# Performance work log

Hardware: AMD Instinct MI355X
Metric: run time of the kernel (lower is better)

The kernel has to match this reference:

```python
import jax, jax.numpy as jnp
import numpy as np

B, N, C = 8, 4096, 768
H = 12
D = C // H  # 64


def setup_inputs() -> dict:
    key = jax.random.key(0)
    k1, k2, k3 = jax.random.split(key, 3)
    x = jax.random.normal(k1, (B, N, C), dtype=jnp.float32)
    Wqkv = jax.random.normal(k2, (C, 3 * C), dtype=jnp.float32) * (1.0 / np.sqrt(C))
    Wproj = jax.random.normal(k3, (C, C), dtype=jnp.float32) * (1.0 / np.sqrt(C))
    bproj = jnp.zeros((C,), dtype=jnp.float32)
    return {"x": x, "Wqkv": Wqkv, "Wproj": Wproj, "bproj": bproj}


def reference(x, Wqkv, Wproj, bproj):
    b, n, c = x.shape
    # qkv: [B,N,3C] -> [B,N,3,H,D] -> [3,B,H,N,D]
    qkv = (x @ Wqkv).reshape(b, n, 3, H, D).transpose(2, 0, 3, 1, 4)
    q, k, v = qkv[0], qkv[1], qkv[2]
    q = jax.nn.softmax(q, axis=-1)  # softmax over head_dim (feature map)
    k = jax.nn.softmax(k, axis=-1)
    # context: [B,H,D,D] (small per-head matrix)
    context = jnp.einsum('bhnd,bhne->bhde', k, v)
    out = jnp.einsum('bhnd,bhde->bhne', q, context)  # [B,H,N,D]
    out = out.transpose(0, 2, 1, 3).reshape(b, n, c)
    return out @ Wproj + bproj
```

## Files before the change

kernel.cpp:

```cpp
#include <hip/hip_runtime.h>

typedef unsigned short u16;
typedef unsigned int u32;
typedef __attribute__((ext_vector_type(4))) float f32x4;
typedef __attribute__((ext_vector_type(8))) short bf16x8;
typedef __attribute__((ext_vector_type(8))) u16 u16x8;

__device__ __forceinline__ u16 f2b(float f) {
  union { float f; u32 u; } v; v.f = f;
  u32 r = v.u + 0x7FFFu + ((v.u >> 16) & 1u);
  return (u16)(r >> 16);
}
__device__ __forceinline__ float b2f(u16 h) {
  union { u32 u; float f; } v; v.u = ((u32)h) << 16;
  return v.f;
}
__device__ __forceinline__ void gload_lds16(const void* g, void* lds) {
  __builtin_amdgcn_global_load_lds(
      (__attribute__((address_space(1))) void*)(void*)g,
      (__attribute__((address_space(3))) void*)lds, 16, 0, 0);
}

__global__ __launch_bounds__(256) void cast_x_kernel(const float* __restrict__ x,
                                                     u16* __restrict__ xb, size_t n8) {
  size_t i = (size_t)blockIdx.x * blockDim.x + threadIdx.x;
  size_t stride = (size_t)gridDim.x * blockDim.x;
  for (; i < n8; i += stride) {
    const float4* p = (const float4*)(x + i * 8);
    float4 a = p[0], b = p[1];
    u16x8 o;
    o[0] = f2b(a.x); o[1] = f2b(a.y); o[2] = f2b(a.z); o[3] = f2b(a.w);
    o[4] = f2b(b.x); o[5] = f2b(b.y); o[6] = f2b(b.z); o[7] = f2b(b.w);
    *(u16x8*)(xb + i * 8) = o;
  }
}

template <bool PERM>
__global__ __launch_bounds__(256) void transpose_cast_kernel(const float* __restrict__ W,
                                                             u16* __restrict__ WT,
                                                             int R, int C) {
  __shared__ u16 tile[32][33];
  int rt = R >> 5;
  int tr = blockIdx.x % rt, tc = blockIdx.x / rt;
  int r0 = tr * 32, c0 = tc * 32;
#pragma unroll
  for (int i = 0; i < 4; ++i) {
    int r = (threadIdx.x >> 5) + i * 8, c = threadIdx.x & 31;
    tile[r][c] = f2b(W[(size_t)(r0 + r) * C + c0 + c]);
  }
  __syncthreads();
#pragma unroll
  for (int i = 0; i < 4; ++i) {
    int c = (threadIdx.x >> 5) + i * 8, r = threadIdx.x & 31;
    int cc = c0 + c;
    if (PERM && cc >= 768) {
      int t = cc - 768;
      int isv = (t >= 768) ? 1 : 0;
      int tk = t - isv * 768;
      cc = 768 + (tk >> 6) * 128 + isv * 64 + (tk & 63);
    }
    WT[(size_t)cc * R + r0 + r] = tile[r][c];
  }
}

template <bool G1, bool BIAS, bool BATCHB>
__global__ __launch_bounds__(256, 4) void gemm128_kernel(
    const u16* __restrict__ A, const u16* __restrict__ BT, void* __restrict__ Cv,
    float* __restrict__ Pw, const float* __restrict__ bias, int N, int lda, int ntile) {
  constexpr int K = 768;
  constexpr int NT = 24;
  __shared__ __align__(16) u16 lds[20480];
  u16* Asb = lds;
  u16* Bsb = lds + 8192;
  const int tid = threadIdx.x;
  const int wave = tid >> 6, lane = tid & 63;
  const int lr = lane & 15, hi = lane >> 4;
  const int wr = wave >> 1, wc = wave & 1;

  const int cpx = gridDim.x >> 3;
  const int wg = (blockIdx.x & 7) * cpx + (blockIdx.x >> 3);
  const int tm = wg / ntile, tn = wg % ntile;

  const size_t rowA0 = (size_t)tm * 128;
  const size_t rowB0 = (size_t)tn * 128;
  const u16* BTb = BATCHB ? (BT + (size_t)(tm >> 5) * 589824) : BT;

  const int dby = tid * 16;
  const int sby = dby ^ (((dby >> 7) & 3) << 4);
  const int srow = sby >> 6;
  const int scol = (sby & 63) >> 1;
  const u16* pA = A + (rowA0 + srow) * (size_t)lda + scol;
  const u16* pB = BTb + (rowB0 + srow) * (size_t)K + scol;
  u16* Adst = Asb + wave * 512;
  u16* Bdst = Bsb + wave * 512;

  const int flip = ((lr >> 1) & 3) << 4;
  const int baseA = ((((wr * 64 + lr) * 64) + hi * 16) ^ flip) >> 1;
  const int baseB = ((((wc * 64 + lr) * 64) + hi * 16) ^ flip) >> 1;

  f32x4 acc[4][4] = {};

#define STG_A(tt)                                                          \
  { const u16* _s = pA + (size_t)(tt) * 32;                                \
    u16* _d = Adst + ((tt) & 1) * 4096;                                    \
    gload_lds16(_s, _d); gload_lds16(_s + (size_t)64 * lda, _d + 2048); }
#define STG_B(tt)                                                          \
  { const u16* _s = pB + (size_t)(tt) * 32;                                \
    u16* _d = Bdst + ((tt) % 3) * 4096;                                    \
    gload_lds16(_s, _d); gload_lds16(_s + (size_t)64 * K, _d + 2048); }

  STG_A(0); STG_B(0); STG_B(1);
  asm volatile("s_waitcnt vmcnt(2)" ::: "memory");
  __builtin_amdgcn_sched_barrier(0);
  __builtin_amdgcn_s_barrier();

#pragma unroll
  for (int t = 0; t < NT; ++t) {
    const u16* Ab = Asb + (t & 1) * 4096;
    const u16* Bb = Bsb + (t % 3) * 4096;
    bf16x8 a0 = *(const bf16x8*)&Ab[baseA];
    bf16x8 a1 = *(const bf16x8*)&Ab[baseA + 512];
    bf16x8 a2 = *(const bf16x8*)&Ab[baseA + 1024];
    bf16x8 a3 = *(const bf16x8*)&Ab[baseA + 1536];
    bf16x8 b0 = *(const bf16x8*)&Bb[baseB];
    bf16x8 b1 = *(const bf16x8*)&Bb[baseB + 512];
    bf16x8 b2 = *(const bf16x8*)&Bb[baseB + 1024];
    bf16x8 b3 = *(const bf16x8*)&Bb[baseB + 1536];
    if (t + 1 < NT) STG_A(t + 1);
    if (t + 2 < NT) STG_B(t + 2);
    asm volatile("s_waitcnt lgkmcnt(0)" ::: "memory");
    __builtin_amdgcn_sched_barrier(0);
    __builtin_amdgcn_s_setprio(1);
    acc[0][0] = __builtin_amdgcn_mfma_f32_16x16x32_bf16(a0, b0, acc[0][0], 0, 0, 0);
    acc[0][1] = __builtin_amdgcn_mfma_f32_16x16x32_bf16(a0, b1, acc[0][1], 0, 0, 0);
    acc[0][2] = __builtin_amdgcn_mfma_f32_16x16x32_bf16(a0, b2, acc[0][2], 0, 0, 0);
    acc[0][3] = __builtin_amdgcn_mfma_f32_16x16x32_bf16(a0, b3, acc[0][3], 0, 0, 0);
    acc[1][0] = __builtin_amdgcn_mfma_f32_16x16x32_bf16(a1, b0, acc[1][0], 0, 0, 0);
    acc[1][1] = __builtin_amdgcn_mfma_f32_16x16x32_bf16(a1, b1, acc[1][1], 0, 0, 0);
    acc[1][2] = __builtin_amdgcn_mfma_f32_16x16x32_bf16(a1, b2, acc[1][2], 0, 0, 0);
    acc[1][3] = __builtin_amdgcn_mfma_f32_16x16x32_bf16(a1, b3, acc[1][3], 0, 0, 0);
    acc[2][0] = __builtin_amdgcn_mfma_f32_16x16x32_bf16(a2, b0, acc[2][0], 0, 0, 0);
    acc[2][1] = __builtin_amdgcn_mfma_f32_16x16x32_bf16(a2, b1, acc[2][1], 0, 0, 0);
    acc[2][2] = __builtin_amdgcn_mfma_f32_16x16x32_bf16(a2, b2, acc[2][2], 0, 0, 0);
    acc[2][3] = __builtin_amdgcn_mfma_f32_16x16x32_bf16(a2, b3, acc[2][3], 0, 0, 0);
    acc[3][0] = __builtin_amdgcn_mfma_f32_16x16x32_bf16(a3, b0, acc[3][0], 0, 0, 0);
    acc[3][1] = __builtin_amdgcn_mfma_f32_16x16x32_bf16(a3, b1, acc[3][1], 0, 0, 0);
    acc[3][2] = __builtin_amdgcn_mfma_f32_16x16x32_bf16(a3, b2, acc[3][2], 0, 0, 0);
    acc[3][3] = __builtin_amdgcn_mfma_f32_16x16x32_bf16(a3, b3, acc[3][3], 0, 0, 0);
    __builtin_amdgcn_s_setprio(0);
    if (t < NT - 2) {
      asm volatile("s_waitcnt vmcnt(2)" ::: "memory");
    } else if (t == NT - 2) {
      asm volatile("s_waitcnt vmcnt(0)" ::: "memory");
    }
    __builtin_amdgcn_sched_barrier(0);
    if (t + 1 < NT) __builtin_amdgcn_s_barrier();
  }
#undef STG_A
#undef STG_B

  const int ocol0 = tn * 128 + wc * 64;
  const int orow0 = tm * 128 + wr * 64;

  if (!G1 || tn < 6) {
#pragma unroll
    for (int mf = 0; mf < 4; ++mf) {
      if (G1) {
#pragma unroll
        for (int q = 0; q < 4; ++q) {
          float v0 = acc[mf][0][q], v1 = acc[mf][1][q];
          float v2 = acc[mf][2][q], v3 = acc[mf][3][q];
          float mx = fmaxf(fmaxf(v0, v1), fmaxf(v2, v3));
#pragma unroll
          for (int s = 1; s <= 8; s <<= 1) mx = fmaxf(mx, __shfl_xor(mx, s, 64));
          float e0 = __expf(v0 - mx), e1 = __expf(v1 - mx);
          float e2 = __expf(v2 - mx), e3 = __expf(v3 - mx);
          float sm = e0 + e1 + e2 + e3;
#pragma unroll
          for (int s = 1; s <= 8; s <<= 1) sm += __shfl_xor(sm, s, 64);
          float inv = 1.0f / sm;
          acc[mf][0][q] = e0 * inv; acc[mf][1][q] = e1 * inv;
          acc[mf][2][q] = e2 * inv; acc[mf][3][q] = e3 * inv;
        }
      }
#pragma unroll
      for (int nf = 0; nf < 4; ++nf) {
        const int col = ocol0 + nf * 16 + lr;
        const float bv = BIAS ? bias[col] : 0.0f;
#pragma unroll
        for (int q = 0; q < 4; ++q) {
          const int row = orow0 + mf * 16 + hi * 4 + q;
          const float v = acc[mf][nf][q] + bv;
          if (G1) ((u16*)Cv)[(size_t)row * 768 + col] = f2b(v);
          else    ((float*)Cv)[(size_t)row * N + col] = v;
        }
      }
    }
  } else {
    const int h = tn - 6;
    if (wc == 0) {
#pragma unroll
      for (int mf = 0; mf < 4; ++mf)
#pragma unroll
        for (int q = 0; q < 4; ++q) {
          float v0 = acc[mf][0][q], v1 = acc[mf][1][q];
          float v2 = acc[mf][2][q], v3 = acc[mf][3][q];
          float mx = fmaxf(fmaxf(v0, v1), fmaxf(v2, v3));
#pragma unroll
          for (int s = 1; s <= 8; s <<= 1) mx = fmaxf(mx, __shfl_xor(mx, s, 64));
          float e0 = __expf(v0 - mx), e1 = __expf(v1 - mx);
          float e2 = __expf(v2 - mx), e3 = __expf(v3 - mx);
          float sm = e0 + e1 + e2 + e3;
#pragma unroll
          for (int s = 1; s <= 8; s <<= 1) sm += __shfl_xor(sm, s, 64);
          float inv = 1.0f / sm;
          acc[mf][0][q] = e0 * inv; acc[mf][1][q] = e1 * inv;
          acc[mf][2][q] = e2 * inv; acc[mf][3][q] = e3 * inv;
        }
    }
    __syncthreads();
    u16* kT = lds;
    u16* vT = lds + 8704;
    u16* tgt = wc ? vT : kT;
#pragma unroll
    for (int mf = 0; mf < 4; ++mf)
#pragma unroll
      for (int nf = 0; nf < 4; ++nf)
#pragma unroll
        for (int q = 0; q < 4; ++q)
          tgt[(nf * 16 + lr) * 136 + wr * 64 + mf * 16 + hi * 4 + q] =
              f2b(acc[mf][nf][q]);
    __syncthreads();
    f32x4 cacc[4] = {};
#pragma unroll
    for (int ks = 0; ks < 4; ++ks) {
      bf16x8 ak = *(const bf16x8*)&kT[(wave * 16 + lr) * 136 + ks * 32 + hi * 8];
#pragma unroll
      for (int ef = 0; ef < 4; ++ef) {
        bf16x8 bv = *(const bf16x8*)&vT[(ef * 16 + lr) * 136 + ks * 32 + hi * 8];
        cacc[ef] = __builtin_amdgcn_mfma_f32_16x16x32_bf16(ak, bv, cacc[ef], 0, 0, 0);
      }
    }
    float* dst = Pw + ((size_t)tm * 12 + h) * 4096;
#pragma unroll
    for (int ef = 0; ef < 4; ++ef)
#pragma unroll
      for (int q = 0; q < 4; ++q)
        dst[(wave * 16 + hi * 4 + q) * 64 + ef * 16 + lr] = cacc[ef][q];
  }
}

__global__ __launch_bounds__(256) void ctx_reduce_kernel(const float* __restrict__ partial,
                                                         u16* __restrict__ ctxD) {
  int idx = blockIdx.x * 256 + threadIdx.x;
  int bh = idx >> 12;
  int b = bh / 12, h = bh % 12;
  int de = idx & 4095;
  float s = 0.0f;
#pragma unroll 8
  for (int i = 0; i < 32; ++i)
    s += partial[((size_t)(b * 32 + i) * 12 + h) * 4096 + de];
  ctxD[(size_t)bh * 4096 + de] = f2b(s);
}

__global__ __launch_bounds__(256) void make_w2_kernel(const u16* __restrict__ WprojT,
                                                      const u16* __restrict__ ctxD,
                                                      u16* __restrict__ BT2) {
  __shared__ u16 qs[128 * 64];
  __shared__ u16 cs[64 * 64];
  int bid = blockIdx.x;
  int b = bid / 72, rest = bid % 72;
  int h = rest / 6, ct = rest % 6;
  int bh = b * 12 + h;
  int tid = threadIdx.x, wave = tid >> 6, lane = tid & 63;
  int lr = lane & 15, lk = (lane >> 4) << 3;
#pragma unroll
  for (int it = 0; it < 4; ++it) {
    int u = it * 256 + tid;
    int r = u >> 3, c8 = (u & 7) * 8;
    gload_lds16(WprojT + (size_t)(ct * 128 + r) * 768 + h * 64 + c8,
                &qs[(it * 256 + wave * 64) * 8]);
  }
#pragma unroll
  for (int it = 0; it < 2; ++it) {
    int u = it * 256 + tid;
    gload_lds16(ctxD + (size_t)bh * 4096 + u * 8, &cs[(it * 256 + wave * 64) * 8]);
  }
  asm volatile("s_waitcnt vmcnt(0)" ::: "memory");
  __syncthreads();
  f32x4 acc[2][4] = {};
#pragma unroll
  for (int ks = 0; ks < 2; ++ks) {
    bf16x8 bv[4];
#pragma unroll
    for (int jt = 0; jt < 4; ++jt) bv[jt] = *(const bf16x8*)&cs[(jt * 16 + lr) * 64 + ks * 32 + lk];
#pragma unroll
    for (int i = 0; i < 2; ++i) {
      bf16x8 af = *(const bf16x8*)&qs[(wave * 32 + i * 16 + lr) * 64 + ks * 32 + lk];
#pragma unroll
      for (int jt = 0; jt < 4; ++jt)
        acc[i][jt] = __builtin_amdgcn_mfma_f32_16x16x32_bf16(af, bv[jt], acc[i][jt], 0, 0, 0);
    }
  }
#pragma unroll
  for (int i = 0; i < 2; ++i)
#pragma unroll
    for (int jt = 0; jt < 4; ++jt)
#pragma unroll
      for (int q = 0; q < 4; ++q) {
        int cp = ct * 128 + wave * 32 + i * 16 + (lane >> 4) * 4 + q;
        int col = h * 64 + jt * 16 + lr;
        BT2[(size_t)b * 589824 + (size_t)cp * 768 + col] = f2b(acc[i][jt][q]);
      }
}

extern "C" void kernel_launch(void* const* d_in, const int* in_sizes, int n_in,
                              void* d_out, int out_size, void* d_ws, size_t ws_size,
                              hipStream_t stream) {
  const float* x = (const float*)d_in[0];
  const float* Wqkv = (const float*)d_in[1];
  const float* Wproj = (const float*)d_in[2];
  const float* bproj = (const float*)d_in[3];
  float* out = (float*)d_out;
  char* ws = (char*)d_ws;

  u16* xb      = (u16*)(ws);
  u16* WqkvT   = (u16*)(ws + 50331648);
  u16* WprojT  = (u16*)(ws + 53870592);
  u16* qbuf    = (u16*)(ws + 55050240);
  float* partial = (float*)(ws + 105381888);
  u16* ctxD    = (u16*)(ws + 155713536);
  u16* BT2     = (u16*)(ws + 156499968);

  cast_x_kernel<<<2048, 256, 0, stream>>>(x, xb, (size_t)(32768ll * 768 / 8));
  transpose_cast_kernel<true><<<(768 / 32) * (2304 / 32), 256, 0, stream>>>(Wqkv, WqkvT, 768, 2304);
  transpose_cast_kernel<false><<<(768 / 32) * (768 / 32), 256, 0, stream>>>(Wproj, WprojT, 768, 768);

  gemm128_kernel<true, false, false><<<(32768 / 128) * (2304 / 128), 256, 0, stream>>>(
      xb, WqkvT, (void*)qbuf, partial, nullptr, 2304, 768, 2304 / 128);

  ctx_reduce_kernel<<<(96 * 4096) / 256, 256, 0, stream>>>(partial, ctxD);
  make_w2_kernel<<<8 * 12 * 6, 256, 0, stream>>>(WprojT, ctxD, BT2);

  gemm128_kernel<false, true, true><<<(32768 / 128) * (768 / 128), 256, 0, stream>>>(
      qbuf, BT2, (void*)out, nullptr, bproj, 768, 768, 768 / 128);
}
```

Before: 283.1 us.

## Load GEMM A operand directly into registers and store context partials as bf16

The GEMM no longer stages the A tile through LDS. Each lane loads its A fragments straight from global memory into double-buffered registers, which shrinks LDS use and drops the A-side LDS traffic, but lowers the occupancy hint from 4 to 3 blocks. The per-tile context partials are now written as bf16 instead of fp32, and the reduction kernel reads 8 values per thread with vector loads. This halves partial-buffer traffic at the cost of some precision in the summed context matrix.

```diff
diff --git a/kernel.cpp b/kernel.cpp
--- a/kernel.cpp
+++ b/kernel.cpp
@@ -64,14 +64,13 @@
 }
 
 template <bool G1, bool BIAS, bool BATCHB>
-__global__ __launch_bounds__(256, 4) void gemm128_kernel(
+__global__ __launch_bounds__(256, 3) void gemm128_kernel(
     const u16* __restrict__ A, const u16* __restrict__ BT, void* __restrict__ Cv,
-    float* __restrict__ Pw, const float* __restrict__ bias, int N, int lda, int ntile) {
+    void* __restrict__ Pw, const float* __restrict__ bias, int N, int lda, int ntile) {
   constexpr int K = 768;
   constexpr int NT = 24;
-  __shared__ __align__(16) u16 lds[20480];
-  u16* Asb = lds;
-  u16* Bsb = lds + 8192;
+  __shared__ __align__(16) u16 lds[17408];
+  u16* Bsb = lds;
   const int tid = threadIdx.x;
   const int wave = tid >> 6, lane = tid & 63;
   const int lr = lane & 15, hi = lane >> 4;
@@ -89,64 +88,64 @@
   const int sby = dby ^ (((dby >> 7) & 3) << 4);
   const int srow = sby >> 6;
   const int scol = (sby & 63) >> 1;
-  const u16* pA = A + (rowA0 + srow) * (size_t)lda + scol;
   const u16* pB = BTb + (rowB0 + srow) * (size_t)K + scol;
-  u16* Adst = Asb + wave * 512;
   u16* Bdst = Bsb + wave * 512;
 
   const int flip = ((lr >> 1) & 3) << 4;
-  const int baseA = ((((wr * 64 + lr) * 64) + hi * 16) ^ flip) >> 1;
   const int baseB = ((((wc * 64 + lr) * 64) + hi * 16) ^ flip) >> 1;
 
+  const u16* pAr[4];
+#pragma unroll
+  for (int mf = 0; mf < 4; ++mf)
+    pAr[mf] = A + (rowA0 + wr * 64 + mf * 16 + lr) * (size_t)lda + hi * 8;
+
   f32x4 acc[4][4] = {};
-
-#define STG_A(tt)                                                          \
-  { const u16* _s = pA + (size_t)(tt) * 32;                                \
-    u16* _d = Adst + ((tt) & 1) * 4096;                                    \
-    gload_lds16(_s, _d); gload_lds16(_s + (size_t)64 * lda, _d + 2048); }
+  bf16x8 areg[2][4];
+
 #define STG_B(tt)                                                          \
   { const u16* _s = pB + (size_t)(tt) * 32;                                \
     u16* _d = Bdst + ((tt) % 3) * 4096;                                    \
     gload_lds16(_s, _d); gload_lds16(_s + (size_t)64 * K, _d + 2048); }
 
-  STG_A(0); STG_B(0); STG_B(1);
+  STG_B(0); STG_B(1);
+#pragma unroll
+  for (int mf = 0; mf < 4; ++mf) areg[0][mf] = *(const bf16x8*)(pAr[mf]);
   asm volatile("s_waitcnt vmcnt(2)" ::: "memory");
   __builtin_amdgcn_sched_barrier(0);
   __builtin_amdgcn_s_barrier();
 
 #pragma unroll
   for (int t = 0; t < NT; ++t) {
-    const u16* Ab = Asb + (t & 1) * 4096;
     const u16* Bb = Bsb + (t % 3) * 4096;
-    bf16x8 a0 = *(const bf16x8*)&Ab[baseA];
-    bf16x8 a1 = *(const bf16x8*)&Ab[baseA + 512];
-    bf16x8 a2 = *(const bf16x8*)&Ab[baseA + 1024];
-    bf16x8 a3 = *(const bf16x8*)&Ab[baseA + 1536];
     bf16x8 b0 = *(const bf16x8*)&Bb[baseB];
     bf16x8 b1 = *(const bf16x8*)&Bb[baseB + 512];
     bf16x8 b2 = *(const bf16x8*)&Bb[baseB + 1024];
     bf16x8 b3 = *(const bf16x8*)&Bb[baseB + 1536];
-    if (t + 1 < NT) STG_A(t + 1);
+    if (t + 1 < NT) {
+#pragma unroll
+      for (int mf = 0; mf < 4; ++mf)
+        areg[(t + 1) & 1][mf] = *(const bf16x8*)(pAr[mf] + (t + 1) * 32);
+    }
     if (t + 2 < NT) STG_B(t + 2);
     asm volatile("s_waitcnt lgkmcnt(0)" ::: "memory");
     __builtin_amdgcn_sched_barrier(0);
     __builtin_amdgcn_s_setprio(1);
-    acc[0][0] = __builtin_amdgcn_mfma_f32_16x16x32_bf16(a0, b0, acc[0][0], 0, 0, 0);
-    acc[0][1] = __builtin_amdgcn_mfma_f32_16x16x32_bf16(a0, b1, acc[0][1], 0, 0, 0);
-    acc[0][2] = __builtin_amdgcn_mfma_f32_16x16x32_bf16(a0, b2, acc[0][2], 0, 0, 0);
-    acc[0][3] = __builtin_amdgcn_mfma_f32_16x16x32_bf16(a0, b3, acc[0][3], 0, 0, 0);
-    acc[1][0] = __builtin_amdgcn_mfma_f32_16x16x32_bf16(a1, b0, acc[1][0], 0, 0, 0);
-    acc[1][1] = __builtin_amdgcn_mfma_f32_16x16x32_bf16(a1, b1, acc[1][1], 0, 0, 0);
-    acc[1][2] = __builtin_amdgcn_mfma_f32_16x16x32_bf16(a1, b2, acc[1][2], 0, 0, 0);
-    acc[1][3] = __builtin_amdgcn_mfma_f32_16x16x32_bf16(a1, b3, acc[1][3], 0, 0, 0);
-    acc[2][0] = __builtin_amdgcn_mfma_f32_16x16x32_bf16(a2, b0, acc[2][0], 0, 0, 0);
-    acc[2][1] = __builtin_amdgcn_mfma_f32_16x16x32_bf16(a2, b1, acc[2][1], 0, 0, 0);
-    acc[2][2] = __builtin_amdgcn_mfma_f32_16x16x32_bf16(a2, b2, acc[2][2], 0, 0, 0);
-    acc[2][3] = __builtin_amdgcn_mfma_f32_16x16x32_bf16(a2, b3, acc[2][3], 0, 0, 0);
-    acc[3][0] = __builtin_amdgcn_mfma_f32_16x16x32_bf16(a3, b0, acc[3][0], 0, 0, 0);
-    acc[3][1] = __builtin_amdgcn_mfma_f32_16x16x32_bf16(a3, b1, acc[3][1], 0, 0, 0);
-    acc[3][2] = __builtin_amdgcn_mfma_f32_16x16x32_bf16(a3, b2, acc[3][2], 0, 0, 0);
-    acc[3][3] = __builtin_amdgcn_mfma_f32_16x16x32_bf16(a3, b3, acc[3][3], 0, 0, 0);
+    acc[0][0] = __builtin_amdgcn_mfma_f32_16x16x32_bf16(areg[t & 1][0], b0, acc[0][0], 0, 0, 0);
+    acc[0][1] = __builtin_amdgcn_mfma_f32_16x16x32_bf16(areg[t & 1][0], b1, acc[0][1], 0, 0, 0);
+    acc[0][2] = __builtin_amdgcn_mfma_f32_16x16x32_bf16(areg[t & 1][0], b2, acc[0][2], 0, 0, 0);
+    acc[0][3] = __builtin_amdgcn_mfma_f32_16x16x32_bf16(areg[t & 1][0], b3, acc[0][3], 0, 0, 0);
+    acc[1][0] = __builtin_amdgcn_mfma_f32_16x16x32_bf16(areg[t & 1][1], b0, acc[1][0], 0, 0, 0);
+    acc[1][1] = __builtin_amdgcn_mfma_f32_16x16x32_bf16(areg[t & 1][1], b1, acc[1][1], 0, 0, 0);
+    acc[1][2] = __builtin_amdgcn_mfma_f32_16x16x32_bf16(areg[t & 1][1], b2, acc[1][2], 0, 0, 0);
+    acc[1][3] = __builtin_amdgcn_mfma_f32_16x16x32_bf16(areg[t & 1][1], b3, acc[1][3], 0, 0, 0);
+    acc[2][0] = __builtin_amdgcn_mfma_f32_16x16x32_bf16(areg[t & 1][2], b0, acc[2][0], 0, 0, 0);
+    acc[2][1] = __builtin_amdgcn_mfma_f32_16x16x32_bf16(areg[t & 1][2], b1, acc[2][1], 0, 0, 0);
+    acc[2][2] = __builtin_amdgcn_mfma_f32_16x16x32_bf16(areg[t & 1][2], b2, acc[2][2], 0, 0, 0);
+    acc[2][3] = __builtin_amdgcn_mfma_f32_16x16x32_bf16(areg[t & 1][2], b3, acc[2][3], 0, 0, 0);
+    acc[3][0] = __builtin_amdgcn_mfma_f32_16x16x32_bf16(areg[t & 1][3], b0, acc[3][0], 0, 0, 0);
+    acc[3][1] = __builtin_amdgcn_mfma_f32_16x16x32_bf16(areg[t & 1][3], b1, acc[3][1], 0, 0, 0);
+    acc[3][2] = __builtin_amdgcn_mfma_f32_16x16x32_bf16(areg[t & 1][3], b2, acc[3][2], 0, 0, 0);
+    acc[3][3] = __builtin_amdgcn_mfma_f32_16x16x32_bf16(areg[t & 1][3], b3, acc[3][3], 0, 0, 0);
     __builtin_amdgcn_s_setprio(0);
     if (t < NT - 2) {
       asm volatile("s_waitcnt vmcnt(2)" ::: "memory");
@@ -156,7 +155,6 @@
     __builtin_amdgcn_sched_barrier(0);
     if (t + 1 < NT) __builtin_amdgcn_s_barrier();
   }
-#undef STG_A
 #undef STG_B
 
   const int ocol0 = tn * 128 + wc * 64;
@@ -241,26 +239,33 @@
         cacc[ef] = __builtin_amdgcn_mfma_f32_16x16x32_bf16(ak, bv, cacc[ef], 0, 0, 0);
       }
     }
-    float* dst = Pw + ((size_t)tm * 12 + h) * 4096;
+    u16* dst = (u16*)Pw + ((size_t)tm * 12 + h) * 4096;
 #pragma unroll
     for (int ef = 0; ef < 4; ++ef)
 #pragma unroll
       for (int q = 0; q < 4; ++q)
-        dst[(wave * 16 + hi * 4 + q) * 64 + ef * 16 + lr] = cacc[ef][q];
-  }
-}
-
-__global__ __launch_bounds__(256) void ctx_reduce_kernel(const float* __restrict__ partial,
+        dst[(wave * 16 + hi * 4 + q) * 64 + ef * 16 + lr] = f2b(cacc[ef][q]);
+  }
+}
+
+__global__ __launch_bounds__(256) void ctx_reduce_kernel(const u16* __restrict__ partial,
                                                          u16* __restrict__ ctxD) {
-  int idx = blockIdx.x * 256 + threadIdx.x;
+  int idx = (blockIdx.x * 256 + threadIdx.x) * 8;
   int bh = idx >> 12;
   int b = bh / 12, h = bh % 12;
   int de = idx & 4095;
-  float s = 0.0f;
-#pragma unroll 8
-  for (int i = 0; i < 32; ++i)
-    s += partial[((size_t)(b * 32 + i) * 12 + h) * 4096 + de];
-  ctxD[(size_t)bh * 4096 + de] = f2b(s);
+  const u16* base = partial + ((size_t)(b * 32) * 12 + h) * 4096 + de;
+  float s[8] = {};
+#pragma unroll 4
+  for (int i = 0; i < 32; ++i) {
+    u16x8 v = *(const u16x8*)(base + (size_t)i * 49152);
+#pragma unroll
+    for (int j = 0; j < 8; ++j) s[j] += b2f(v[j]);
+  }
+  u16x8 o;
+#pragma unroll
+  for (int j = 0; j < 8; ++j) o[j] = f2b(s[j]);
+  *(u16x8*)(ctxD + (size_t)bh * 4096 + de) = o;
 }
 
 __global__ __launch_bounds__(256) void make_w2_kernel(const u16* __restrict__ WprojT,
@@ -328,18 +333,18 @@
   u16* WqkvT   = (u16*)(ws + 50331648);
   u16* WprojT  = (u16*)(ws + 53870592);
   u16* qbuf    = (u16*)(ws + 55050240);
-  float* partial = (float*)(ws + 105381888);
-  u16* ctxD    = (u16*)(ws + 155713536);
-  u16* BT2     = (u16*)(ws + 156499968);
+  u16* partial = (u16*)(ws + 105381888);
+  u16* ctxD    = (u16*)(ws + 130547712);
+  u16* BT2     = (u16*)(ws + 131334144);
 
   cast_x_kernel<<<2048, 256, 0, stream>>>(x, xb, (size_t)(32768ll * 768 / 8));
   transpose_cast_kernel<true><<<(768 / 32) * (2304 / 32), 256, 0, stream>>>(Wqkv, WqkvT, 768, 2304);
   transpose_cast_kernel<false><<<(768 / 32) * (768 / 32), 256, 0, stream>>>(Wproj, WprojT, 768, 768);
 
   gemm128_kernel<true, false, false><<<(32768 / 128) * (2304 / 128), 256, 0, stream>>>(
-      xb, WqkvT, (void*)qbuf, partial, nullptr, 2304, 768, 2304 / 128);
-
-  ctx_reduce_kernel<<<(96 * 4096) / 256, 256, 0, stream>>>(partial, ctxD);
+      xb, WqkvT, (void*)qbuf, (void*)partial, nullptr, 2304, 768, 2304 / 128);
+
+  ctx_reduce_kernel<<<(96 * 4096) / (256 * 8), 256, 0, stream>>>(partial, ctxD);
   make_w2_kernel<<<8 * 12 * 6, 256, 0, stream>>>(WprojT, ctxD, BT2);
 
   gemm128_kernel<false, true, true><<<(32768 / 128) * (768 / 128), 256, 0, stream>>>(
```

New measurement: 370.8 us. 30.9% more time.

## Stage GEMM1 epilogue through LDS for vectorized stores, store context partials as bf16

Applied to the files above, without the earlier changes.

The q-softmax epilogue now writes bf16 results to a per-wave LDS tile and then issues 16-byte coalesced global stores instead of scattered 2-byte stores. The per-tile K^T V context partials are converted to bf16 and also written through LDS with vector stores. The reduce kernel reads them as bf16 with 8-wide vector loads, which halves the partial buffer traffic. The cost is extra LDS round-trips and barriers in the epilogue, plus some precision loss because partials are rounded to bf16 before summation.

```diff
diff --git a/kernel.cpp b/kernel.cpp
--- a/kernel.cpp
+++ b/kernel.cpp
@@ -66,7 +66,7 @@
 template <bool G1, bool BIAS, bool BATCHB>
 __global__ __launch_bounds__(256, 4) void gemm128_kernel(
     const u16* __restrict__ A, const u16* __restrict__ BT, void* __restrict__ Cv,
-    float* __restrict__ Pw, const float* __restrict__ bias, int N, int lda, int ntile) {
+    void* __restrict__ Pw, const float* __restrict__ bias, int N, int lda, int ntile) {
   constexpr int K = 768;
   constexpr int NT = 24;
   __shared__ __align__(16) u16 lds[20480];
@@ -162,10 +162,56 @@
   const int ocol0 = tn * 128 + wc * 64;
   const int orow0 = tm * 128 + wr * 64;
 
-  if (!G1 || tn < 6) {
+  if (!G1) {
+#pragma unroll
+    for (int mf = 0; mf < 4; ++mf)
+#pragma unroll
+      for (int nf = 0; nf < 4; ++nf) {
+        const int col = ocol0 + nf * 16 + lr;
+        const float bv = BIAS ? bias[col] : 0.0f;
+#pragma unroll
+        for (int q = 0; q < 4; ++q) {
+          const int row = orow0 + mf * 16 + hi * 4 + q;
+          ((float*)Cv)[(size_t)row * N + col] = acc[mf][nf][q] + bv;
+        }
+      }
+  } else if (tn < 6) {
+    __syncthreads();
+    u16* wlds = lds + wave * 4352;
 #pragma unroll
     for (int mf = 0; mf < 4; ++mf) {
-      if (G1) {
+#pragma unroll
+      for (int q = 0; q < 4; ++q) {
+        float v0 = acc[mf][0][q], v1 = acc[mf][1][q];
+        float v2 = acc[mf][2][q], v3 = acc[mf][3][q];
+        float mx = fmaxf(fmaxf(v0, v1), fmaxf(v2, v3));
+#pragma unroll
+        for (int s = 1; s <= 8; s <<= 1) mx = fmaxf(mx, __shfl_xor(mx, s, 64));
+        float e0 = __expf(v0 - mx), e1 = __expf(v1 - mx);
+        float e2 = __expf(v2 - mx), e3 = __expf(v3 - mx);
+        float sm = e0 + e1 + e2 + e3;
+#pragma unroll
+        for (int s = 1; s <= 8; s <<= 1) sm += __shfl_xor(sm, s, 64);
+        float inv = 1.0f / sm;
+        const int rw = mf * 16 + hi * 4 + q;
+        wlds[rw * 68 + 0 * 16 + lr] = f2b(e0 * inv);
+        wlds[rw * 68 + 1 * 16 + lr] = f2b(e1 * inv);
+        wlds[rw * 68 + 2 * 16 + lr] = f2b(e2 * inv);
+        wlds[rw * 68 + 3 * 16 + lr] = f2b(e3 * inv);
+      }
+    }
+#pragma unroll
+    for (int it = 0; it < 8; ++it) {
+      const int row = it * 8 + (lane >> 3);
+      const int c8 = (lane & 7) * 8;
+      u16x8 v = *(const u16x8*)&wlds[row * 68 + c8];
+      *(u16x8*)((u16*)Cv + (size_t)(orow0 + row) * 768 + ocol0 + c8) = v;
+    }
+  } else {
+    const int h = tn - 6;
+    if (wc == 0) {
+#pragma unroll
+      for (int mf = 0; mf < 4; ++mf)
 #pragma unroll
         for (int q = 0; q < 4; ++q) {
           float v0 = acc[mf][0][q], v1 = acc[mf][1][q];
@@ -182,41 +228,6 @@
           acc[mf][0][q] = e0 * inv; acc[mf][1][q] = e1 * inv;
           acc[mf][2][q] = e2 * inv; acc[mf][3][q] = e3 * inv;
         }
-      }
-#pragma unroll
-      for (int nf = 0; nf < 4; ++nf) {
-        const int col = ocol0 + nf * 16 + lr;
-        const float bv = BIAS ? bias[col] : 0.0f;
-#pragma unroll
-        for (int q = 0; q < 4; ++q) {
-          const int row = orow0 + mf * 16 + hi * 4 + q;
-          const float v = acc[mf][nf][q] + bv;
-          if (G1) ((u16*)Cv)[(size_t)row * 768 + col] = f2b(v);
-          else    ((float*)Cv)[(size_t)row * N + col] = v;
-        }
-      }
-    }
-  } else {
-    const int h = tn - 6;
-    if (wc == 0) {
-#pragma unroll
-      for (int mf = 0; mf < 4; ++mf)
-#pragma unroll
-        for (int q = 0; q < 4; ++q) {
-          float v0 = acc[mf][0][q], v1 = acc[mf][1][q];
-          float v2 = acc[mf][2][q], v3 = acc[mf][3][q];
-          float mx = fmaxf(fmaxf(v0, v1), fmaxf(v2, v3));
-#pragma unroll
-          for (int s = 1; s <= 8; s <<= 1) mx = fmaxf(mx, __shfl_xor(mx, s, 64));
-          float e0 = __expf(v0 - mx), e1 = __expf(v1 - mx);
-          float e2 = __expf(v2 - mx), e3 = __expf(v3 - mx);
-          float sm = e0 + e1 + e2 + e3;
-#pragma unroll
-          for (int s = 1; s <= 8; s <<= 1) sm += __shfl_xor(sm, s, 64);
-          float inv = 1.0f / sm;
-          acc[mf][0][q] = e0 * inv; acc[mf][1][q] = e1 * inv;
-          acc[mf][2][q] = e2 * inv; acc[mf][3][q] = e3 * inv;
-        }
     }
     __syncthreads();
     u16* kT = lds;
@@ -241,26 +252,43 @@
         cacc[ef] = __builtin_amdgcn_mfma_f32_16x16x32_bf16(ak, bv, cacc[ef], 0, 0, 0);
       }
     }
-    float* dst = Pw + ((size_t)tm * 12 + h) * 4096;
+    __syncthreads();
+    u16* blds = lds;
 #pragma unroll
     for (int ef = 0; ef < 4; ++ef)
 #pragma unroll
       for (int q = 0; q < 4; ++q)
-        dst[(wave * 16 + hi * 4 + q) * 64 + ef * 16 + lr] = cacc[ef][q];
-  }
-}
-
-__global__ __launch_bounds__(256) void ctx_reduce_kernel(const float* __restrict__ partial,
+        blds[(wave * 16 + hi * 4 + q) * 68 + ef * 16 + lr] = f2b(cacc[ef][q]);
+    __syncthreads();
+    u16* pdst = (u16*)Pw + ((size_t)tm * 12 + h) * 4096;
+#pragma unroll
+    for (int it = 0; it < 2; ++it) {
+      const int seg = it * 256 + tid;
+      const int row = seg >> 3, c8 = (seg & 7) * 8;
+      u16x8 v = *(const u16x8*)&blds[row * 68 + c8];
+      *(u16x8*)(pdst + row * 64 + c8) = v;
+    }
+  }
+}
+
+__global__ __launch_bounds__(256) void ctx_reduce_kernel(const u16* __restrict__ partial,
                                                          u16* __restrict__ ctxD) {
-  int idx = blockIdx.x * 256 + threadIdx.x;
+  int idx = (blockIdx.x * 256 + threadIdx.x) * 8;
   int bh = idx >> 12;
   int b = bh / 12, h = bh % 12;
   int de = idx & 4095;
-  float s = 0.0f;
-#pragma unroll 8
-  for (int i = 0; i < 32; ++i)
-    s += partial[((size_t)(b * 32 + i) * 12 + h) * 4096 + de];
-  ctxD[(size_t)bh * 4096 + de] = f2b(s);
+  const u16* base = partial + ((size_t)(b * 32) * 12 + h) * 4096 + de;
+  float s[8] = {};
+#pragma unroll 4
+  for (int i = 0; i < 32; ++i) {
+    u16x8 v = *(const u16x8*)(base + (size_t)i * 49152);
+#pragma unroll
+    for (int j = 0; j < 8; ++j) s[j] += b2f(v[j]);
+  }
+  u16x8 o;
+#pragma unroll
+  for (int j = 0; j < 8; ++j) o[j] = f2b(s[j]);
+  *(u16x8*)(ctxD + (size_t)bh * 4096 + de) = o;
 }
 
 __global__ __launch_bounds__(256) void make_w2_kernel(const u16* __restrict__ WprojT,
@@ -328,18 +356,18 @@
   u16* WqkvT   = (u16*)(ws + 50331648);
   u16* WprojT  = (u16*)(ws + 53870592);
   u16* qbuf    = (u16*)(ws + 55050240);
-  float* partial = (float*)(ws + 105381888);
-  u16* ctxD    = (u16*)(ws + 155713536);
-  u16* BT2     = (u16*)(ws + 156499968);
+  u16* partial = (u16*)(ws + 105381888);
+  u16* ctxD    = (u16*)(ws + 130547712);
+  u16* BT2     = (u16*)(ws + 131334144);
 
   cast_x_kernel<<<2048, 256, 0, stream>>>(x, xb, (size_t)(32768ll * 768 / 8));
   transpose_cast_kernel<true><<<(768 / 32) * (2304 / 32), 256, 0, stream>>>(Wqkv, WqkvT, 768, 2304);
   transpose_cast_kernel<false><<<(768 / 32) * (768 / 32), 256, 0, stream>>>(Wproj, WprojT, 768, 768);
 
   gemm128_kernel<true, false, false><<<(32768 / 128) * (2304 / 128), 256, 0, stream>>>(
-      xb, WqkvT, (void*)qbuf, partial, nullptr, 2304, 768, 2304 / 128);
-
-  ctx_reduce_kernel<<<(96 * 4096) / 256, 256, 0, stream>>>(partial, ctxD);
+      xb, WqkvT, (void*)qbuf, (void*)partial, nullptr, 2304, 768, 2304 / 128);
+
+  ctx_reduce_kernel<<<(96 * 4096) / (256 * 8), 256, 0, stream>>>(partial, ctxD);
   make_w2_kernel<<<8 * 12 * 6, 256, 0, stream>>>(WprojT, ctxD, BT2);
 
   gemm128_kernel<false, true, true><<<(32768 / 128) * (768 / 128), 256, 0, stream>>>(
```

New measurement: 270.0 us (median of 2 runs). 4.6% less time.
